# Performance work log

Hardware: AMD Instinct MI355X
Metric: run time of the kernel (lower is better)

The kernel has to match this reference:

```python
import jax, jax.numpy as jnp
import numpy as np
import math

TIME_DIM = 32

def fourier_time_embedding(t, time_dim=TIME_DIM):
    # Sinusoidal Fourier features of scalar t -> [time_dim]
    half = time_dim // 2
    freqs = jnp.exp(-math.log(10000.0) * jnp.arange(half, dtype=jnp.float32) / half)
    args = t * freqs
    return jnp.concatenate([jnp.sin(args), jnp.cos(args)], axis=-1)


def setup_inputs() -> dict:
    key = jax.random.key(0)
    kh, ka, kw1, kb1, kw2, kb2 = jax.random.split(key, 6)
    B, C, D, T = 16, 1024, 256, 9
    h0 = jax.random.normal(kh, (B, C, D), dtype=jnp.float32)
    time_grid = jnp.arange(T, dtype=jnp.float32)
    adjacency = jax.random.uniform(ka, (B, C, C), dtype=jnp.float32)
    in_dim = 2 * D + TIME_DIM  # 544
    s1 = 1.0 / math.sqrt(in_dim)
    s2 = 1.0 / math.sqrt(D)
    W1 = jax.random.uniform(kw1, (in_dim, D), jnp.float32, -s1, s1)
    b1 = jax.random.uniform(kb1, (D,), jnp.float32, -s1, s1)
    W2 = jax.random.uniform(kw2, (D, D), jnp.float32, -s2, s2)
    b2 = jax.random.uniform(kb2, (D,), jnp.float32, -s2, s2)
    return {"h0": h0, "time_grid": time_grid, "adjacency": adjacency,
            "W1": W1, "b1": b1, "W2": W2, "b2": b2}


def reference(h0, time_grid, adjacency, W1, b1, W2, b2):
    B, C, D = h0.shape
    # adjacency is [B,C,C] (time-constant branch); degree-normalize once
    degree = jnp.clip(adjacency.sum(-1, keepdims=True), 1.0, None)
    adj_norm = adjacency / degree

    def vector_field(t, h):
        agg = jnp.einsum('bij,bjd->bid', adj_norm, h)           # [B,C,D]
        te = fourier_time_embedding(t)                           # [TIME_DIM]
        te_b = jnp.broadcast_to(te, (B, C, TIME_DIM))
        x = jnp.concatenate([h, agg, te_b], axis=-1)             # [B,C,2D+time]
        return jnp.tanh(x @ W1 + b1) @ W2 + b2                   # [B,C,D]

    def rk4_step(h, ts):
        t0, t1 = ts
        dt = t1 - t0
        k1 = vector_field(t0, h)
        k2 = vector_field(t0 + dt / 2, h + dt * k1 / 2)
        k3 = vector_field(t0 + dt / 2, h + dt * k2 / 2)
        k4 = vector_field(t0 + dt, h + dt * k3)
        h_new = h + dt * (k1 + 2 * k2 + 2 * k3 + k4) / 6
        return h_new, h_new

    ts_pairs = jnp.stack([time_grid[:-1], time_grid[1:]], axis=-1)  # [T-1,2]
    _, states = jax.lax.scan(rk4_step, h0, ts_pairs)                 # [T-1,B,C,D]
    traj = jnp.concatenate([h0[None], states], axis=0)               # [T,B,C,D]
    return jnp.transpose(traj, (1, 0, 2, 3))                         # [B,T,C,D]
```

## Files before the change

kernel.cpp:

```cpp
#include <hip/hip_runtime.h>
#include <math.h>

#define NB   16
#define NC   1024
#define ND   256
#define NT_  9
#define TDIM 32

typedef _Float16 half8 __attribute__((ext_vector_type(8)));
typedef _Float16 half4v __attribute__((ext_vector_type(4)));
typedef float f32x4 __attribute__((ext_vector_type(4)));

#define GLL(gp, lp)                                                            \
  __builtin_amdgcn_global_load_lds(                                            \
      (const __attribute__((address_space(1))) void*)(gp),                     \
      (__attribute__((address_space(3))) void*)(lp), 16, 0, 0)

#define MFMA16(A, B, C) __builtin_amdgcn_mfma_f32_16x16x32_f16(A, B, C, 0, 0, 0)


__global__ __launch_bounds__(256) void k_copy_h0(const float* __restrict__ h0,
                                                 float* __restrict__ out) {
  size_t idx = (size_t)blockIdx.x * blockDim.x + threadIdx.x;
  size_t fe = idx * 4;
  size_t b = fe / ((size_t)NC * ND);
  size_t rem = fe % ((size_t)NC * ND);
  float4 v = *(const float4*)(h0 + fe);
  *(float4*)(out + (b * NT_) * (size_t)NC * ND + rem) = v;
}

__global__ __launch_bounds__(256) void k_deg(const float* __restrict__ adj,
                                             float* __restrict__ invdeg) {
  int wave = threadIdx.x >> 6;
  int lane = threadIdx.x & 63;
  int row = blockIdx.x * 4 + wave;
  const float* p = adj + (size_t)row * NC;
  float s = 0.f;
#pragma unroll
  for (int q = 0; q < 4; ++q) {
    float4 v = *(const float4*)(p + q * 256 + lane * 4);
    s += v.x + v.y + v.z + v.w;
  }
#pragma unroll
  for (int off = 32; off; off >>= 1) s += __shfl_down(s, off);
  if (lane == 0) invdeg[row] = 1.f / fmaxf(s, 1.f);
}

__global__ __launch_bounds__(256) void k_split_adj(const float* __restrict__ adj,
                                                   _Float16* __restrict__ adjT) {
  int i = blockIdx.x * 256 + threadIdx.x;
  int k0 = (i & 255) * 4;
  int c = (i >> 8) & 1023;
  int b = i >> 18;
  float4 v = *(const float4*)(adj + (((size_t)b * NC + c) << 10) + k0);
  half4v h;
  h[0] = (_Float16)v.x; h[1] = (_Float16)v.y;
  h[2] = (_Float16)v.z; h[3] = (_Float16)v.w;
  int mq = c >> 5, t = k0 >> 5;
  size_t base = ((((size_t)b * 32 + mq) * 32) + t) * 1024;
  int chunk = ((k0 & 31) >> 3) * 32 + (c & 31);
  *(half4v*)(adjT + base + chunk * 8 + (k0 & 7)) = h;
}

__global__ __launch_bounds__(256) void k_split_w(const float* __restrict__ W1,
                                                 const float* __restrict__ W2,
                                                 _Float16* __restrict__ W1Tt,
                                                 _Float16* __restrict__ W2Tt) {
  int blk = blockIdx.x;
  int tid = threadIdx.x;
  if (blk < 128) {
    int i = blk * 256 + tid;
    int n = i & 255, k0 = (i >> 8) * 4;
    half4v h;
#pragma unroll
    for (int q = 0; q < 4; ++q) h[q] = (_Float16)W1[(size_t)(k0 + q) * ND + n];
    int t = k0 >> 5;
    int chunk = ((k0 & 31) >> 3) * 256 + n;
    *(half4v*)(W1Tt + (size_t)t * 8192 + chunk * 8 + (k0 & 7)) = h;
  } else {
    int i = (blk - 128) * 256 + tid;
    int n = i & 255, k0 = (i >> 8) * 4;
    half4v h;
#pragma unroll
    for (int q = 0; q < 4; ++q) h[q] = (_Float16)W2[(size_t)(k0 + q) * ND + n];
    int t = k0 >> 5;
    int chunk = ((k0 & 31) >> 3) * 256 + n;
    *(half4v*)(W2Tt + (size_t)t * 8192 + chunk * 8 + (k0 & 7)) = h;
  }
}

__global__ __launch_bounds__(256) void k_htsplit(const float* __restrict__ src,
                                                 _Float16* __restrict__ hHt,
                                                 _Float16* __restrict__ hLt,
                                                 _Float16* __restrict__ hTt) {
  int i = blockIdx.x * 256 + threadIdx.x;
  int d0 = (i & 63) * 4;
  int c = (i >> 6) & 1023;
  int b = i >> 16;
  float4 v = *(const float4*)(src + (((size_t)b * NC + c) << 8) + d0);
  float vv[4] = {v.x, v.y, v.z, v.w};
  half4v hh, ll;
#pragma unroll
  for (int q = 0; q < 4; ++q) {
    _Float16 h = (_Float16)vv[q];
    hh[q] = h;
    ll[q] = (_Float16)(vv[q] - (float)h);
  }
  int mq = c >> 5, ta = d0 >> 5;
  size_t abase = ((((size_t)b * 32 + mq) * 8) + ta) * 1024;
  int achunk = ((d0 & 31) >> 3) * 32 + (c & 31);
  *(half4v*)(hHt + abase + achunk * 8 + (d0 & 7)) = hh;
  *(half4v*)(hLt + abase + achunk * 8 + (d0 & 7)) = ll;
  size_t tbase = ((size_t)b * 32 + mq) * 8192;
  int gk = (c & 31) >> 3, offc = c & 7;
#pragma unroll
  for (int q = 0; q < 4; ++q)
    hTt[tbase + (size_t)(gk * 256 + d0 + q) * 8 + offc] = hh[q];
}

__global__ __launch_bounds__(512, 4) void k_stage(
    const _Float16* __restrict__ adjT,
    _Float16* __restrict__ hHt, _Float16* __restrict__ hLt,
    const _Float16* __restrict__ hTr, _Float16* __restrict__ hTw,
    const float* __restrict__ invdeg,
    const _Float16* __restrict__ W1Tt, const _Float16* __restrict__ W2Tt,
    const float* __restrict__ W1, const float* __restrict__ b1,
    const float* __restrict__ b2, const float* __restrict__ tg,
    int step, int stage, float* __restrict__ out, float* __restrict__ accws) {
  __shared__ __align__(16) _Float16 Bs[2][8192];
  __shared__ __align__(16) _Float16 As[2][2048];
  __shared__ __align__(16) _Float16 POOL[8192];
  __shared__ float te_s[TDIM];
  __shared__ float b1s[256];
  _Float16* aggS = POOL;
  _Float16* uS = POOL;

  const int tid = threadIdx.x;
  const int lane = tid & 63, wid = tid >> 6;
  const int g = lane >> 4, r = lane & 15, rg = (lane >> 4) * 4;
  const int p = blockIdx.x;
  const int b = ((p >> 3) >> 5) * 8 + (p & 7);
  const int mq = (p >> 3) & 31;

  const _Float16* adjB = adjT + (((size_t)b * 32 + mq) * 32) * 1024;
  const _Float16* hTb = hTr + (size_t)b * 32 * 8192;
  const _Float16* hHb = hHt + (((size_t)b * 32 + mq) * 8) * 1024;
  const _Float16* hLb = hLt + (((size_t)b * 32 + mq) * 8) * 1024;

  f32x4 acc[2][2] = {};

#define STAGE_B(SRC, DST)                                                      \
  do {                                                                         \
    GLL((SRC) + (size_t)tid * 8, (DST) + (size_t)tid * 8);                     \
    GLL((SRC) + (size_t)(512 + tid) * 8, (DST) + (size_t)(512 + tid) * 8);     \
  } while (0)

#define STAGE_A1(SRC, DST)                                                     \
  do {                                                                         \
    if (tid < 128) GLL((SRC) + (size_t)tid * 8, (DST) + (size_t)tid * 8);      \
  } while (0)

#define STAGE_AHL(TA, DST)                                                     \
  do {                                                                         \
    if (tid < 128)                                                             \
      GLL(hHb + (size_t)(TA) * 1024 + tid * 8, (DST) + (size_t)tid * 8);       \
    else if (tid < 256)                                                        \
      GLL(hLb + (size_t)(TA) * 1024 + (tid - 128) * 8,                         \
          (DST) + 1024 + (size_t)(tid - 128) * 8);                             \
  } while (0)

  STAGE_A1(adjB, As[0]);
  STAGE_B(hTb, Bs[0]);
  if (tid < 16) {
    float t0 = tg[step], t1 = tg[step + 1];
    float frac = (stage == 0) ? 0.f : ((stage == 3) ? 1.f : 0.5f);
    float t = t0 + frac * (t1 - t0);
    float f = expf(-logf(10000.f) * (float)tid / 16.f);
    te_s[tid] = sinf(t * f);
    te_s[tid + 16] = cosf(t * f);
  }
  __syncthreads();
  if (tid < 256) {
    float s = b1[tid];
#pragma unroll
    for (int q = 0; q < TDIM; ++q)
      s = fmaf(te_s[q], W1[(size_t)(512 + q) * ND + tid], s);
    b1s[tid] = s;
  }

  for (int t = 0; t < 32; ++t) {
    int cur = t & 1;
    if (t < 31) {
      STAGE_A1(adjB + (size_t)(t + 1) * 1024, As[cur ^ 1]);
      STAGE_B(hTb + (size_t)(t + 1) * 8192, Bs[cur ^ 1]);
    } else {
      STAGE_AHL(0, As[cur ^ 1]);
      STAGE_B(W1Tt, Bs[cur ^ 1]);
    }
    half8 Af[2], Bf[2];
#pragma unroll
    for (int i = 0; i < 2; ++i)
      Af[i] = ((const half8*)As[cur])[g * 32 + i * 16 + r];
#pragma unroll
    for (int j = 0; j < 2; ++j)
      Bf[j] = ((const half8*)Bs[cur])[g * 256 + wid * 32 + j * 16 + r];
#pragma unroll
    for (int i = 0; i < 2; ++i)
#pragma unroll
      for (int j = 0; j < 2; ++j) acc[i][j] = MFMA16(Af[i], Bf[j], acc[i][j]);
    __syncthreads();
  }
#pragma unroll
  for (int i = 0; i < 2; ++i) {
#pragma unroll
    for (int j = 0; j < 2; ++j) {
      int d = wid * 32 + j * 16 + r;
#pragma unroll
      for (int q = 0; q < 4; ++q) {
        int lr = i * 16 + rg + q;
        float v = acc[i][j][q] * invdeg[b * NC + mq * 32 + lr];
        aggS[((d >> 3) * 32 + lr) * 8 + (d & 7)] = (_Float16)v;
      }
      acc[i][j] = (f32x4){0.f, 0.f, 0.f, 0.f};
    }
  }
  __syncthreads();

  for (int t = 0; t < 16; ++t) {
    int cur = t & 1;
    if (t < 15) {
      if (t + 1 < 8) STAGE_AHL(t + 1, As[cur ^ 1]);
      STAGE_B(W1Tt + (size_t)(t + 1) * 8192, Bs[cur ^ 1]);
    } else {
      STAGE_B(W2Tt, Bs[cur ^ 1]);
    }
    half8 AH[2], AL[2], Bf[2];
    const bool hasL = (t < 8);
    if (hasL) {
#pragma unroll
      for (int i = 0; i < 2; ++i) {
        AH[i] = ((const half8*)As[cur])[g * 32 + i * 16 + r];
        AL[i] = ((const half8*)(As[cur] + 1024))[g * 32 + i * 16 + r];
      }
    } else {
#pragma unroll
      for (int i = 0; i < 2; ++i)
        AH[i] = ((const half8*)aggS)[((t - 8) * 4 + g) * 32 + i * 16 + r];
    }
#pragma unroll
    for (int j = 0; j < 2; ++j)
      Bf[j] = ((const half8*)Bs[cur])[g * 256 + wid * 32 + j * 16 + r];
#pragma unroll
    for (int i = 0; i < 2; ++i)
#pragma unroll
      for (int j = 0; j < 2; ++j) {
        acc[i][j] = MFMA16(AH[i], Bf[j], acc[i][j]);
        if (hasL) acc[i][j] = MFMA16(AL[i], Bf[j], acc[i][j]);
      }
    __syncthreads();
  }
#pragma unroll
  for (int i = 0; i < 2; ++i) {
#pragma unroll
    for (int j = 0; j < 2; ++j) {
      int col = wid * 32 + j * 16 + r;
#pragma unroll
      for (int q = 0; q < 4; ++q) {
        int row = i * 16 + rg + q;
        float v = tanhf(acc[i][j][q] + b1s[col]);
        uS[((col >> 3) * 32 + row) * 8 + (col & 7)] = (_Float16)v;
      }
      acc[i][j] = (f32x4){0.f, 0.f, 0.f, 0.f};
    }
  }
  __syncthreads();

  for (int t = 0; t < 8; ++t) {
    int cur = t & 1;
    if (t < 7) STAGE_B(W2Tt + (size_t)(t + 1) * 8192, Bs[cur ^ 1]);
    half8 Af[2], Bf[2];
#pragma unroll
    for (int i = 0; i < 2; ++i)
      Af[i] = ((const half8*)uS)[(t * 4 + g) * 32 + i * 16 + r];
#pragma unroll
    for (int j = 0; j < 2; ++j)
      Bf[j] = ((const half8*)Bs[cur])[g * 256 + wid * 32 + j * 16 + r];
#pragma unroll
    for (int i = 0; i < 2; ++i)
#pragma unroll
      for (int j = 0; j < 2; ++j) acc[i][j] = MFMA16(Af[i], Bf[j], acc[i][j]);
    __syncthreads();
  }
  const float t0 = tg[step], t1 = tg[step + 1];
  const float dt = t1 - t0;
  const float cs = (stage == 2) ? dt : 0.5f * dt;
#pragma unroll
  for (int i = 0; i < 2; ++i) {
#pragma unroll
    for (int j = 0; j < 2; ++j) {
      int col = wid * 32 + j * 16 + r;
      float bb2 = b2[col];
      int ii0 = mq * 32 + i * 16 + rg;
      size_t hrow = (((size_t)b * NT_ + step) * NC + ii0) * (size_t)ND + col;
      size_t wrow = ((size_t)b * NC + ii0) * (size_t)ND + col;
      float val[4];
#pragma unroll
      for (int q = 0; q < 4; ++q) {
        float f = acc[i][j][q] + bb2;
        float hb = out[hrow + (size_t)q * ND];
        size_t widx = wrow + (size_t)q * ND;
        if (stage == 0) {
          accws[widx] = f;
          val[q] = hb + cs * f;
        } else if (stage == 3) {
          float hn = hb + (dt / 6.f) * (accws[widx] + f);
          out[hrow + (size_t)NC * ND + (size_t)q * ND] = hn;
          val[q] = hn;
        } else {
          accws[widx] += 2.f * f;
          val[q] = hb + cs * f;
        }
      }
      half4v th, tl;
#pragma unroll
      for (int q = 0; q < 4; ++q) {
        _Float16 hh = (_Float16)val[q];
        th[q] = hh;
        tl[q] = (_Float16)(val[q] - (float)hh);
      }
      int ta = col >> 5;
      size_t hbase = (((size_t)b * 32 + mq) * 8 + ta) * 1024;
      int cb = ((col & 31) >> 3) * 32 + (ii0 & 31);
      int offc = col & 7;
#pragma unroll
      for (int q = 0; q < 4; ++q) {
        hHt[hbase + (size_t)(cb + q) * 8 + offc] = th[q];
        hLt[hbase + (size_t)(cb + q) * 8 + offc] = tl[q];
      }
      size_t tbase = ((size_t)b * 32 + mq) * 8192;
      int gk = (ii0 & 31) >> 3;
      *(half4v*)(hTw + tbase + (size_t)(gk * 256 + col) * 8 + (ii0 & 7)) = th;
    }
  }
#undef STAGE_B
#undef STAGE_A1
#undef STAGE_AHL
}

extern "C" void kernel_launch(void* const* d_in, const int* in_sizes, int n_in,
                              void* d_out, int out_size, void* d_ws, size_t ws_size,
                              hipStream_t stream) {
  const float* h0 = (const float*)d_in[0];
  const float* tg = (const float*)d_in[1];
  const float* adj = (const float*)d_in[2];
  const float* W1 = (const float*)d_in[3];
  const float* b1 = (const float*)d_in[4];
  const float* W2 = (const float*)d_in[5];
  const float* b2 = (const float*)d_in[6];
  float* out = (float*)d_out;

  const size_t CD = (size_t)NC * ND;
  char* w = (char*)d_ws;
  float* invdeg = (float*)w;     w += (size_t)16384 * 4;
  float* accws = (float*)w;      w += (size_t)NB * CD * 4;
  _Float16* adjT = (_Float16*)w; w += (size_t)NB * NC * NC * 2;
  _Float16* hHt = (_Float16*)w;  w += (size_t)NB * CD * 2;
  _Float16* hLt = (_Float16*)w;  w += (size_t)NB * CD * 2;
  _Float16* hTa = (_Float16*)w;  w += (size_t)NB * CD * 2;
  _Float16* hTb = (_Float16*)w;  w += (size_t)NB * CD * 2;
  _Float16* W1Tt = (_Float16*)w; w += (size_t)256 * 512 * 2;
  _Float16* W2Tt = (_Float16*)w; w += (size_t)256 * 256 * 2;

  k_copy_h0<<<dim3(4096), dim3(256), 0, stream>>>(h0, out);
  k_deg<<<dim3(4096), dim3(256), 0, stream>>>(adj, invdeg);
  k_split_adj<<<dim3(16384), dim3(256), 0, stream>>>(adj, adjT);
  k_split_w<<<dim3(192), dim3(256), 0, stream>>>(W1, W2, W1Tt, W2Tt);
  k_htsplit<<<dim3(4096), dim3(256), 0, stream>>>(h0, hHt, hLt, hTa);

  int par = 0;
  for (int s = 0; s < NT_ - 1; ++s) {
    for (int st = 0; st < 4; ++st) {
      k_stage<<<dim3(512), dim3(512), 0, stream>>>(
          adjT, hHt, hLt, par ? hTb : hTa, par ? hTa : hTb, invdeg, W1Tt, W2Tt,
          W1, b1, b2, tg, s, st, out, accws);
      par ^= 1;
    }
  }
}
```

Baseline: 1.664 ms.

## Split fused stage kernel into separate aggregation GEMM and MLP kernels

The fused per-stage kernel computed adjacency aggregation with a 32-row by 256-column tile, so every block re-read the full h slab for its batch. Aggregation now runs in its own kernel with 128x64 output tiles and writes the aggregate to global memory in fp16. The MLP kernel then streams that aggregate like the h tiles. The larger tiles are meant to cut redundant h traffic and raise MFMA reuse, at the cost of a second launch per stage and an extra round trip of the aggregate through global memory.

Result: slower. 1.893 ms (+13.7%).

```diff
diff --git a/kernel.cpp b/kernel.cpp
--- a/kernel.cpp
+++ b/kernel.cpp
@@ -118,22 +118,98 @@
     hTt[tbase + (size_t)(gk * 256 + d0 + q) * 8 + offc] = hh[q];
 }
 
-__global__ __launch_bounds__(512, 4) void k_stage(
-    const _Float16* __restrict__ adjT,
+__global__ __launch_bounds__(256) void k_agg(const _Float16* __restrict__ adjT,
+                                             const _Float16* __restrict__ hTt,
+                                             const float* __restrict__ invdeg,
+                                             _Float16* __restrict__ aggT) {
+  __shared__ __align__(16) _Float16 As[2][4096];
+  __shared__ __align__(16) _Float16 Bs[2][2048];
+  const int tid = threadIdx.x;
+  const int lane = tid & 63, wid = tid >> 6;
+  const int wm = wid >> 1, wn = wid & 1;
+  const int g = lane >> 4, r = lane & 15, rg = (lane >> 4) * 4;
+  const int p = blockIdx.x;
+  const int b = ((p >> 3) >> 5) * 8 + (p & 7);
+  const int q32 = (p >> 3) & 31;
+  const int m_t = q32 >> 2, n_t = q32 & 3;
+  const int m0 = m_t * 128, n0 = n_t * 64;
+
+  f32x4 acc[4][2] = {};
+
+#define STAGE_A(T, DST)                                                        \
+  do {                                                                         \
+    _Pragma("unroll") for (int c2 = 0; c2 < 2; ++c2) {                         \
+      int e = c2 * 256 + tid;                                                  \
+      int qq = e >> 7, ch = e & 127;                                           \
+      GLL(adjT + ((((size_t)b * 32 + (m0 >> 5) + qq) * 32) + (T)) * 1024 +     \
+              ch * 8,                                                          \
+          (DST) + (size_t)e * 8);                                              \
+    }                                                                          \
+  } while (0)
+
+#define STAGE_Bh(T, DST)                                                       \
+  do {                                                                         \
+    int gk = tid >> 6, nn = tid & 63;                                          \
+    GLL(hTt + ((size_t)b * 32 + (T)) * 8192 + (size_t)(gk * 256 + n0 + nn) * 8,\
+        (DST) + (size_t)tid * 8);                                              \
+  } while (0)
+
+  STAGE_A(0, As[0]);
+  STAGE_Bh(0, Bs[0]);
+  __syncthreads();
+  for (int t = 0; t < 32; ++t) {
+    int cur = t & 1;
+    if (t < 31) {
+      STAGE_A(t + 1, As[cur ^ 1]);
+      STAGE_Bh(t + 1, Bs[cur ^ 1]);
+    }
+    half8 Af[4], Bf[2];
+#pragma unroll
+    for (int i = 0; i < 4; ++i) {
+      int row = wm * 64 + i * 16 + r;
+      Af[i] = ((const half8*)As[cur])[((row >> 5) * 4 + g) * 32 + (row & 31)];
+    }
+#pragma unroll
+    for (int j = 0; j < 2; ++j)
+      Bf[j] = ((const half8*)Bs[cur])[g * 64 + wn * 32 + j * 16 + r];
+#pragma unroll
+    for (int i = 0; i < 4; ++i)
+#pragma unroll
+      for (int j = 0; j < 2; ++j) acc[i][j] = MFMA16(Af[i], Bf[j], acc[i][j]);
+    __syncthreads();
+  }
+#pragma unroll
+  for (int i = 0; i < 4; ++i) {
+#pragma unroll
+    for (int j = 0; j < 2; ++j) {
+      int col = n0 + wn * 32 + j * 16 + r;
+      int ta = col >> 5;
+      int cgk = (col & 31) >> 3, offc = col & 7;
+#pragma unroll
+      for (int q = 0; q < 4; ++q) {
+        int m = m0 + wm * 64 + i * 16 + rg + q;
+        float v = acc[i][j][q] * invdeg[b * NC + m];
+        size_t base = (((size_t)b * 32 + (m >> 5)) * 8 + ta) * 1024;
+        aggT[base + (size_t)(cgk * 32 + (m & 31)) * 8 + offc] = (_Float16)v;
+      }
+    }
+  }
+#undef STAGE_A
+#undef STAGE_Bh
+}
+
+__global__ __launch_bounds__(512, 4) void k_mlp(
     _Float16* __restrict__ hHt, _Float16* __restrict__ hLt,
-    const _Float16* __restrict__ hTr, _Float16* __restrict__ hTw,
-    const float* __restrict__ invdeg,
+    const _Float16* __restrict__ aggT, _Float16* __restrict__ hTw,
     const _Float16* __restrict__ W1Tt, const _Float16* __restrict__ W2Tt,
     const float* __restrict__ W1, const float* __restrict__ b1,
     const float* __restrict__ b2, const float* __restrict__ tg,
     int step, int stage, float* __restrict__ out, float* __restrict__ accws) {
   __shared__ __align__(16) _Float16 Bs[2][8192];
   __shared__ __align__(16) _Float16 As[2][2048];
-  __shared__ __align__(16) _Float16 POOL[8192];
+  __shared__ __align__(16) _Float16 uS[8192];
   __shared__ float te_s[TDIM];
   __shared__ float b1s[256];
-  _Float16* aggS = POOL;
-  _Float16* uS = POOL;
 
   const int tid = threadIdx.x;
   const int lane = tid & 63, wid = tid >> 6;
@@ -142,10 +218,9 @@
   const int b = ((p >> 3) >> 5) * 8 + (p & 7);
   const int mq = (p >> 3) & 31;
 
-  const _Float16* adjB = adjT + (((size_t)b * 32 + mq) * 32) * 1024;
-  const _Float16* hTb = hTr + (size_t)b * 32 * 8192;
   const _Float16* hHb = hHt + (((size_t)b * 32 + mq) * 8) * 1024;
   const _Float16* hLb = hLt + (((size_t)b * 32 + mq) * 8) * 1024;
+  const _Float16* aggB = aggT + (((size_t)b * 32 + mq) * 8) * 1024;
 
   f32x4 acc[2][2] = {};
 
@@ -153,11 +228,6 @@
   do {                                                                         \
     GLL((SRC) + (size_t)tid * 8, (DST) + (size_t)tid * 8);                     \
     GLL((SRC) + (size_t)(512 + tid) * 8, (DST) + (size_t)(512 + tid) * 8);     \
-  } while (0)
-
-#define STAGE_A1(SRC, DST)                                                     \
-  do {                                                                         \
-    if (tid < 128) GLL((SRC) + (size_t)tid * 8, (DST) + (size_t)tid * 8);      \
   } while (0)
 
 #define STAGE_AHL(TA, DST)                                                     \
@@ -169,8 +239,14 @@
           (DST) + 1024 + (size_t)(tid - 128) * 8);                             \
   } while (0)
 
-  STAGE_A1(adjB, As[0]);
-  STAGE_B(hTb, Bs[0]);
+#define STAGE_AGG(TA, DST)                                                     \
+  do {                                                                         \
+    if (tid < 128)                                                             \
+      GLL(aggB + (size_t)(TA) * 1024 + tid * 8, (DST) + (size_t)tid * 8);      \
+  } while (0)
+
+  STAGE_AHL(0, As[0]);
+  STAGE_B(W1Tt, Bs[0]);
   if (tid < 16) {
     float t0 = tg[step], t1 = tg[step + 1];
     float frac = (stage == 0) ? 0.f : ((stage == 3) ? 1.f : 0.5f);
@@ -188,64 +264,21 @@
     b1s[tid] = s;
   }
 
-  for (int t = 0; t < 32; ++t) {
-    int cur = t & 1;
-    if (t < 31) {
-      STAGE_A1(adjB + (size_t)(t + 1) * 1024, As[cur ^ 1]);
-      STAGE_B(hTb + (size_t)(t + 1) * 8192, Bs[cur ^ 1]);
-    } else {
-      STAGE_AHL(0, As[cur ^ 1]);
-      STAGE_B(W1Tt, Bs[cur ^ 1]);
-    }
-    half8 Af[2], Bf[2];
-#pragma unroll
-    for (int i = 0; i < 2; ++i)
-      Af[i] = ((const half8*)As[cur])[g * 32 + i * 16 + r];
-#pragma unroll
-    for (int j = 0; j < 2; ++j)
-      Bf[j] = ((const half8*)Bs[cur])[g * 256 + wid * 32 + j * 16 + r];
-#pragma unroll
-    for (int i = 0; i < 2; ++i)
-#pragma unroll
-      for (int j = 0; j < 2; ++j) acc[i][j] = MFMA16(Af[i], Bf[j], acc[i][j]);
-    __syncthreads();
-  }
-#pragma unroll
-  for (int i = 0; i < 2; ++i) {
-#pragma unroll
-    for (int j = 0; j < 2; ++j) {
-      int d = wid * 32 + j * 16 + r;
-#pragma unroll
-      for (int q = 0; q < 4; ++q) {
-        int lr = i * 16 + rg + q;
-        float v = acc[i][j][q] * invdeg[b * NC + mq * 32 + lr];
-        aggS[((d >> 3) * 32 + lr) * 8 + (d & 7)] = (_Float16)v;
-      }
-      acc[i][j] = (f32x4){0.f, 0.f, 0.f, 0.f};
-    }
-  }
-  __syncthreads();
-
   for (int t = 0; t < 16; ++t) {
     int cur = t & 1;
     if (t < 15) {
       if (t + 1 < 8) STAGE_AHL(t + 1, As[cur ^ 1]);
+      else STAGE_AGG(t + 1 - 8, As[cur ^ 1]);
       STAGE_B(W1Tt + (size_t)(t + 1) * 8192, Bs[cur ^ 1]);
     } else {
       STAGE_B(W2Tt, Bs[cur ^ 1]);
     }
     half8 AH[2], AL[2], Bf[2];
     const bool hasL = (t < 8);
-    if (hasL) {
-#pragma unroll
-      for (int i = 0; i < 2; ++i) {
-        AH[i] = ((const half8*)As[cur])[g * 32 + i * 16 + r];
-        AL[i] = ((const half8*)(As[cur] + 1024))[g * 32 + i * 16 + r];
-      }
-    } else {
-#pragma unroll
-      for (int i = 0; i < 2; ++i)
-        AH[i] = ((const half8*)aggS)[((t - 8) * 4 + g) * 32 + i * 16 + r];
+#pragma unroll
+    for (int i = 0; i < 2; ++i) {
+      AH[i] = ((const half8*)As[cur])[g * 32 + i * 16 + r];
+      AL[i] = ((const half8*)(As[cur] + 1024))[g * 32 + i * 16 + r];
     }
 #pragma unroll
     for (int j = 0; j < 2; ++j)
@@ -343,8 +376,8 @@
     }
   }
 #undef STAGE_B
-#undef STAGE_A1
 #undef STAGE_AHL
+#undef STAGE_AGG
 }
 
 extern "C" void kernel_launch(void* const* d_in, const int* in_sizes, int n_in,
@@ -368,6 +401,7 @@
   _Float16* hLt = (_Float16*)w;  w += (size_t)NB * CD * 2;
   _Float16* hTa = (_Float16*)w;  w += (size_t)NB * CD * 2;
   _Float16* hTb = (_Float16*)w;  w += (size_t)NB * CD * 2;
+  _Float16* aggT = (_Float16*)w; w += (size_t)NB * CD * 2;
   _Float16* W1Tt = (_Float16*)w; w += (size_t)256 * 512 * 2;
   _Float16* W2Tt = (_Float16*)w; w += (size_t)256 * 256 * 2;
 
@@ -380,9 +414,11 @@
   int par = 0;
   for (int s = 0; s < NT_ - 1; ++s) {
     for (int st = 0; st < 4; ++st) {
-      k_stage<<<dim3(512), dim3(512), 0, stream>>>(
-          adjT, hHt, hLt, par ? hTb : hTa, par ? hTa : hTb, invdeg, W1Tt, W2Tt,
-          W1, b1, b2, tg, s, st, out, accws);
+      _Float16* hTr = par ? hTb : hTa;
+      _Float16* hTn = par ? hTa : hTb;
+      k_agg<<<dim3(512), dim3(256), 0, stream>>>(adjT, hTr, invdeg, aggT);
+      k_mlp<<<dim3(512), dim3(512), 0, stream>>>(hHt, hLt, aggT, hTn, W1Tt, W2Tt,
+                                                 W1, b1, b2, tg, s, st, out, accws);
       par ^= 1;
     }
   }
```

## Triple-buffer stage kernel loads with explicit vmcnt waits and split barriers

Applied to the files above, without the earlier changes.

Replaces the double-buffered LDS staging in the fused stage kernel with a three-slot ring that issues loads two iterations ahead through a unified issue schedule covering all three GEMM phases. Full __syncthreads are replaced by an s_waitcnt vmcnt(N) plus s_barrier at the top of each iteration and a bare barrier at the end, so a load can stay in flight across a whole iteration. A-tile loads become 4-byte direct-to-LDS loads spread over all threads, and the inverse degree values are hoisted into registers at kernel start. LDS use rises by one extra buffer, which may reduce occupancy. The hand-tuned vmcnt counts must match the number of loads issued per thread exactly, or data races result.

After: 1.571 ms (median of 2 runs). 5.6% less time.

```diff
diff --git a/kernel.cpp b/kernel.cpp
--- a/kernel.cpp
+++ b/kernel.cpp
@@ -16,7 +16,35 @@
       (const __attribute__((address_space(1))) void*)(gp),                     \
       (__attribute__((address_space(3))) void*)(lp), 16, 0, 0)
 
+#define GLL4(gp, lp)                                                           \
+  __builtin_amdgcn_global_load_lds(                                            \
+      (const __attribute__((address_space(1))) void*)(gp),                     \
+      (__attribute__((address_space(3))) void*)(lp), 4, 0, 0)
+
 #define MFMA16(A, B, C) __builtin_amdgcn_mfma_f32_16x16x32_f16(A, B, C, 0, 0, 0)
+
+#define VBAR(N)                                                                \
+  do {                                                                         \
+    asm volatile("s_waitcnt vmcnt(" #N ")" ::: "memory");                      \
+    __builtin_amdgcn_s_barrier();                                              \
+    asm volatile("" ::: "memory");                                             \
+    __builtin_amdgcn_sched_barrier(0);                                         \
+  } while (0)
+
+#define BAR2()                                                                 \
+  do {                                                                         \
+    asm volatile("" ::: "memory");                                             \
+    __builtin_amdgcn_s_barrier();                                              \
+    asm volatile("" ::: "memory");                                             \
+  } while (0)
+
+#define LBAR()                                                                 \
+  do {                                                                         \
+    asm volatile("s_waitcnt lgkmcnt(0)" ::: "memory");                         \
+    __builtin_amdgcn_s_barrier();                                              \
+    asm volatile("" ::: "memory");                                             \
+    __builtin_amdgcn_sched_barrier(0);                                         \
+  } while (0)
 
 
 __global__ __launch_bounds__(256) void k_copy_h0(const float* __restrict__ h0,
@@ -127,8 +155,8 @@
     const float* __restrict__ W1, const float* __restrict__ b1,
     const float* __restrict__ b2, const float* __restrict__ tg,
     int step, int stage, float* __restrict__ out, float* __restrict__ accws) {
-  __shared__ __align__(16) _Float16 Bs[2][8192];
-  __shared__ __align__(16) _Float16 As[2][2048];
+  __shared__ __align__(16) _Float16 Bs3[3][8192];
+  __shared__ __align__(16) _Float16 As3[3][2048];
   __shared__ __align__(16) _Float16 POOL[8192];
   __shared__ float te_s[TDIM];
   __shared__ float b1s[256];
@@ -149,28 +177,38 @@
 
   f32x4 acc[2][2] = {};
 
+  float iv[2][4];
+#pragma unroll
+  for (int i = 0; i < 2; ++i)
+#pragma unroll
+    for (int q = 0; q < 4; ++q)
+      iv[i][q] = invdeg[b * NC + mq * 32 + i * 16 + rg + q];
+
 #define STAGE_B(SRC, DST)                                                      \
   do {                                                                         \
     GLL((SRC) + (size_t)tid * 8, (DST) + (size_t)tid * 8);                     \
     GLL((SRC) + (size_t)(512 + tid) * 8, (DST) + (size_t)(512 + tid) * 8);     \
   } while (0)
 
-#define STAGE_A1(SRC, DST)                                                     \
-  do {                                                                         \
-    if (tid < 128) GLL((SRC) + (size_t)tid * 8, (DST) + (size_t)tid * 8);      \
-  } while (0)
-
-#define STAGE_AHL(TA, DST)                                                     \
-  do {                                                                         \
-    if (tid < 128)                                                             \
-      GLL(hHb + (size_t)(TA) * 1024 + tid * 8, (DST) + (size_t)tid * 8);       \
-    else if (tid < 256)                                                        \
-      GLL(hLb + (size_t)(TA) * 1024 + (tid - 128) * 8,                         \
-          (DST) + 1024 + (size_t)(tid - 128) * 8);                             \
-  } while (0)
-
-  STAGE_A1(adjB, As[0]);
-  STAGE_B(hTb, Bs[0]);
+  auto issue = [&](int S2) {
+    if (S2 < 32) {
+      GLL4(adjB + (size_t)S2 * 1024 + tid * 2, As3[S2 % 3] + (size_t)tid * 2);
+      STAGE_B(hTb + (size_t)S2 * 8192, Bs3[S2 % 3]);
+    } else if (S2 < 48) {
+      int ta = S2 - 32;
+      if (ta < 8) {
+        GLL4(hHb + (size_t)ta * 1024 + tid * 2, As3[S2 % 3] + (size_t)tid * 2);
+        GLL4(hLb + (size_t)ta * 1024 + tid * 2,
+             As3[S2 % 3] + 1024 + (size_t)tid * 2);
+      }
+      STAGE_B(W1Tt + (size_t)ta * 8192, Bs3[S2 % 3]);
+    } else if (S2 < 56) {
+      STAGE_B(W2Tt + (size_t)(S2 - 48) * 8192, Bs3[S2 % 3]);
+    }
+  };
+
+  issue(0);
+  issue(1);
   if (tid < 16) {
     float t0 = tg[step], t1 = tg[step + 1];
     float frac = (stage == 0) ? 0.f : ((stage == 3) ? 1.f : 0.5f);
@@ -179,7 +217,7 @@
     te_s[tid] = sinf(t * f);
     te_s[tid + 16] = cosf(t * f);
   }
-  __syncthreads();
+  LBAR();
   if (tid < 256) {
     float s = b1[tid];
 #pragma unroll
@@ -189,26 +227,23 @@
   }
 
   for (int t = 0; t < 32; ++t) {
-    int cur = t & 1;
-    if (t < 31) {
-      STAGE_A1(adjB + (size_t)(t + 1) * 1024, As[cur ^ 1]);
-      STAGE_B(hTb + (size_t)(t + 1) * 8192, Bs[cur ^ 1]);
-    } else {
-      STAGE_AHL(0, As[cur ^ 1]);
-      STAGE_B(W1Tt, Bs[cur ^ 1]);
-    }
+    int cur = t % 3;
+    issue(t + 2);
+    if (t < 30) VBAR(6);
+    else if (t == 30) VBAR(7);
+    else VBAR(8);
     half8 Af[2], Bf[2];
 #pragma unroll
     for (int i = 0; i < 2; ++i)
-      Af[i] = ((const half8*)As[cur])[g * 32 + i * 16 + r];
+      Af[i] = ((const half8*)As3[cur])[g * 32 + i * 16 + r];
 #pragma unroll
     for (int j = 0; j < 2; ++j)
-      Bf[j] = ((const half8*)Bs[cur])[g * 256 + wid * 32 + j * 16 + r];
+      Bf[j] = ((const half8*)Bs3[cur])[g * 256 + wid * 32 + j * 16 + r];
 #pragma unroll
     for (int i = 0; i < 2; ++i)
 #pragma unroll
       for (int j = 0; j < 2; ++j) acc[i][j] = MFMA16(Af[i], Bf[j], acc[i][j]);
-    __syncthreads();
+    BAR2();
   }
 #pragma unroll
   for (int i = 0; i < 2; ++i) {
@@ -218,38 +253,37 @@
 #pragma unroll
       for (int q = 0; q < 4; ++q) {
         int lr = i * 16 + rg + q;
-        float v = acc[i][j][q] * invdeg[b * NC + mq * 32 + lr];
+        float v = acc[i][j][q] * iv[i][q];
         aggS[((d >> 3) * 32 + lr) * 8 + (d & 7)] = (_Float16)v;
       }
       acc[i][j] = (f32x4){0.f, 0.f, 0.f, 0.f};
     }
   }
-  __syncthreads();
-
-  for (int t = 0; t < 16; ++t) {
-    int cur = t & 1;
-    if (t < 15) {
-      if (t + 1 < 8) STAGE_AHL(t + 1, As[cur ^ 1]);
-      STAGE_B(W1Tt + (size_t)(t + 1) * 8192, Bs[cur ^ 1]);
+  LBAR();
+
+  for (int ta = 0; ta < 16; ++ta) {
+    int S = 32 + ta;
+    int cur = S % 3;
+    issue(S + 2);
+    if (ta < 6) VBAR(8);
+    else if (ta == 6) VBAR(6);
+    else VBAR(4);
+    half8 AH[2], AL[2], Bf[2];
+    const bool hasL = (ta < 8);
+    if (hasL) {
+#pragma unroll
+      for (int i = 0; i < 2; ++i) {
+        AH[i] = ((const half8*)As3[cur])[g * 32 + i * 16 + r];
+        AL[i] = ((const half8*)(As3[cur] + 1024))[g * 32 + i * 16 + r];
+      }
     } else {
-      STAGE_B(W2Tt, Bs[cur ^ 1]);
-    }
-    half8 AH[2], AL[2], Bf[2];
-    const bool hasL = (t < 8);
-    if (hasL) {
-#pragma unroll
-      for (int i = 0; i < 2; ++i) {
-        AH[i] = ((const half8*)As[cur])[g * 32 + i * 16 + r];
-        AL[i] = ((const half8*)(As[cur] + 1024))[g * 32 + i * 16 + r];
-      }
-    } else {
 #pragma unroll
       for (int i = 0; i < 2; ++i)
-        AH[i] = ((const half8*)aggS)[((t - 8) * 4 + g) * 32 + i * 16 + r];
+        AH[i] = ((const half8*)aggS)[((ta - 8) * 4 + g) * 32 + i * 16 + r];
     }
 #pragma unroll
     for (int j = 0; j < 2; ++j)
-      Bf[j] = ((const half8*)Bs[cur])[g * 256 + wid * 32 + j * 16 + r];
+      Bf[j] = ((const half8*)Bs3[cur])[g * 256 + wid * 32 + j * 16 + r];
 #pragma unroll
     for (int i = 0; i < 2; ++i)
 #pragma unroll
@@ -257,7 +291,7 @@
         acc[i][j] = MFMA16(AH[i], Bf[j], acc[i][j]);
         if (hasL) acc[i][j] = MFMA16(AL[i], Bf[j], acc[i][j]);
       }
-    __syncthreads();
+    BAR2();
   }
 #pragma unroll
   for (int i = 0; i < 2; ++i) {
@@ -273,23 +307,27 @@
       acc[i][j] = (f32x4){0.f, 0.f, 0.f, 0.f};
     }
   }
-  __syncthreads();
-
-  for (int t = 0; t < 8; ++t) {
-    int cur = t & 1;
-    if (t < 7) STAGE_B(W2Tt + (size_t)(t + 1) * 8192, Bs[cur ^ 1]);
+  LBAR();
+
+  for (int tb = 0; tb < 8; ++tb) {
+    int S = 48 + tb;
+    int cur = S % 3;
+    issue(S + 2);
+    if (tb < 6) VBAR(4);
+    else if (tb == 6) VBAR(2);
+    else VBAR(0);
     half8 Af[2], Bf[2];
 #pragma unroll
     for (int i = 0; i < 2; ++i)
-      Af[i] = ((const half8*)uS)[(t * 4 + g) * 32 + i * 16 + r];
+      Af[i] = ((const half8*)uS)[(tb * 4 + g) * 32 + i * 16 + r];
 #pragma unroll
     for (int j = 0; j < 2; ++j)
-      Bf[j] = ((const half8*)Bs[cur])[g * 256 + wid * 32 + j * 16 + r];
+      Bf[j] = ((const half8*)Bs3[cur])[g * 256 + wid * 32 + j * 16 + r];
 #pragma unroll
     for (int i = 0; i < 2; ++i)
 #pragma unroll
       for (int j = 0; j < 2; ++j) acc[i][j] = MFMA16(Af[i], Bf[j], acc[i][j]);
-    __syncthreads();
+    BAR2();
   }
   const float t0 = tg[step], t1 = tg[step + 1];
   const float dt = t1 - t0;
@@ -343,8 +381,6 @@
     }
   }
 #undef STAGE_B
-#undef STAGE_A1
-#undef STAGE_AHL
 }
 
 extern "C" void kernel_launch(void* const* d_in, const int* in_sizes, int n_in,
```
